# Optimization experiments

Hardware: AMD Instinct MI355X
Metric: run time of the kernel (lower is better)

The kernel has to match this reference:

```python
import jax, jax.numpy as jnp
import numpy as np

B, T, C, L = 128, 512, 1024, 64
BLANK = C - 1          # keras ctc_batch_cost uses last class as blank
NEG = -1e9             # finite log-zero (grad-safe)
EPS = 1e-7             # keras.backend.epsilon()


def setup_inputs() -> dict:
    key = jax.random.key(0)
    k1, k2, k3, k4 = jax.random.split(key, 4)
    # y_pred: softmax probabilities, as ctc_batch_cost expects
    y_pred = jax.nn.softmax(jax.random.normal(k1, (B, T, C), dtype=jnp.float32), axis=-1)
    y_true = jax.random.randint(k2, (B, L), 0, BLANK).astype(jnp.int32)  # labels exclude blank
    input_length = jax.random.randint(k3, (B, 1), T // 2, T + 1).astype(jnp.int32)
    label_length = jax.random.randint(k4, (B, 1), L // 2, L + 1).astype(jnp.int32)
    return {"y_true": y_true, "y_pred": y_pred,
            "input_length": input_length, "label_length": label_length}


def _lse3(a, b, c):
    m = jnp.maximum(jnp.maximum(a, b), c)
    return m + jnp.log(jnp.exp(a - m) + jnp.exp(b - m) + jnp.exp(c - m))


def _ctc_loss(y_pred, y_true, input_length, label_length):
    # log probs, exactly as keras: log(y_pred + epsilon)
    logp = jnp.log(y_pred + EPS)                     # [B,T,C]
    Bsz, Tmax, _ = logp.shape
    Lm = y_true.shape[1]
    S = 2 * Lm + 1                                   # extended label length

    # extended labels: blank at even positions, labels at odd
    lab_ext = jnp.full((Bsz, S), BLANK, dtype=y_true.dtype).at[:, 1::2].set(y_true)
    s_idx = jnp.arange(S)
    in_len = input_length.reshape(-1)                # [B]
    lab_len = label_length.reshape(-1)               # [B]
    valid = s_idx[None, :] < (2 * lab_len[:, None] + 1)

    # skip transition s-2 -> s allowed iff lab[s] != blank and lab[s] != lab[s-2]
    lab_m2 = jnp.concatenate(
        [jnp.full((Bsz, 2), -1, dtype=lab_ext.dtype), lab_ext[:, :-2]], axis=1)
    skip_ok = (s_idx[None, :] >= 2) & (lab_ext != BLANK) & (lab_ext != lab_m2)

    # virtual alpha_{-1}: mass only at position 0
    alpha0 = jnp.broadcast_to(jnp.where(s_idx == 0, 0.0, NEG), (Bsz, S)).astype(logp.dtype)

    def step(alpha, inputs):
        lp_t, t = inputs                              # lp_t: [B,C]
        emit = jnp.take_along_axis(lp_t, lab_ext, axis=1)           # [B,S]
        s1 = jnp.concatenate([jnp.full((Bsz, 1), NEG, logp.dtype), alpha[:, :-1]], axis=1)
        s2 = jnp.concatenate([jnp.full((Bsz, 2), NEG, logp.dtype), alpha[:, :-2]], axis=1)
        s2 = jnp.where(skip_ok, s2, NEG)
        a = emit + _lse3(alpha, s1, s2)
        a = jnp.where(valid, a, NEG)
        # freeze alpha once t >= input_length (per-example variable T)
        a = jnp.where((t < in_len)[:, None], a, alpha)
        return a, None

    lp_tb = jnp.transpose(logp, (1, 0, 2))            # [T,B,C]
    alpha_T, _ = jax.lax.scan(step, alpha0, (lp_tb, jnp.arange(Tmax)))

    end_blank = 2 * lab_len                           # index of final blank
    end_label = 2 * lab_len - 1                       # index of final label
    a1 = jnp.take_along_axis(alpha_T, end_blank[:, None], axis=1)[:, 0]
    a2 = jnp.take_along_axis(alpha_T, end_label[:, None], axis=1)[:, 0]
    loss = -jnp.logaddexp(a1, a2)                     # [B]
    return loss[:, None]                              # keras returns [B,1]


def reference(y_true, y_pred, input_length, label_length):
    return _ctc_loss(y_pred, y_true, input_length, label_length)
```

## Files before the change

kernel.cpp:

```cpp
#include <hip/hip_runtime.h>


constexpr int Tmax   = 512;
constexpr int Cch    = 1024;
constexpr int Lm     = 64;
constexpr int BLANKC = Cch - 1;
constexpr int ES     = 65;
constexpr int TS     = 8;
constexpr int PF2    = 8;

#define NEGF (-1e9f)
#define EPSF (1e-7f)
#define LN2F (0.69314718055994530942f)

__device__ __forceinline__ float wave_shr1(float src, float fill) {
    int r = __builtin_amdgcn_update_dpp(__float_as_int(fill), __float_as_int(src),
                                        0x138, 0xf, 0xf, false);
    return __int_as_float(r);
}
__device__ __forceinline__ float lae2(float a, float b) {
    float m = fmaxf(a, b);
    return m + __builtin_log2f(__builtin_exp2f(a - m) + __builtin_exp2f(b - m));
}
__device__ __forceinline__ float lse3_2(float a, float b, float c) {
    float m = fmaxf(fmaxf(a, b), c);
    return m + __builtin_log2f(__builtin_exp2f(a - m) +
                               __builtin_exp2f(b - m) +
                               __builtin_exp2f(c - m));
}
__device__ __forceinline__ int clampi(int v, int lo, int hi) {
    return v < lo ? lo : (v > hi ? hi : v);
}

__global__ __launch_bounds__(64, 1) void ctc_emit(
    const int*   __restrict__ y_true,
    const float* __restrict__ y_pred,
    const int*   __restrict__ in_len,
    float*       __restrict__ E)
{
    const int lane = threadIdx.x;
    const int b    = blockIdx.x;
    const int t0   = blockIdx.y * TS;

    const int Tb = clampi(in_len[b], 0, Tmax);
    if (t0 >= Tb) return;
    const int nt = (Tb - t0) < TS ? (Tb - t0) : TS;

    const int cls = y_true[b * Lm + lane];
    const float* __restrict__ base = y_pred + (size_t)b * Tmax * Cch;

    float pc[TS], pb[TS];
#pragma unroll
    for (int i = 0; i < TS; ++i) {
        const int t = t0 + (i < nt ? i : (nt - 1));
        const float* row = base + (size_t)t * Cch;
        pc[i] = row[cls];
        pb[i] = row[BLANKC];
    }
#pragma unroll
    for (int i = 0; i < TS; ++i) {
        if (i >= nt) break;
        const size_t idx = ((size_t)b * Tmax + (t0 + i)) * ES;
        E[idx + lane] = __builtin_log2f(pc[i] + EPSF);
        if (lane == 0) E[idx + 64] = __builtin_log2f(pb[i] + EPSF);
    }
}

__global__ __launch_bounds__(64, 1) void ctc_rec(
    const int*   __restrict__ y_true,
    const int*   __restrict__ in_len,
    const int*   __restrict__ lab_len,
    const float* __restrict__ E,
    float*       __restrict__ out)
{
    const int b    = blockIdx.x;
    const int lane = threadIdx.x;

    const int cls = y_true[b * Lm + lane];
    const int Tb  = clampi(in_len[b], 0, Tmax);
    const int lb  = clampi(lab_len[b], 0, Lm);

    const int  cls_prev = __shfl_up(cls, 1, 64);
    const bool skip     = (lane >= 1) && (cls != cls_prev);

    const bool val_lo = (lane <= lb);
    const bool val_hi = (lane <  lb);
    const bool val_ex = (lb == Lm);

    float a_lo = (lane == 0) ? 0.f : NEGF;
    float a_hi = NEGF;
    float a_ex = NEGF;

    const float* __restrict__ eb = E + (size_t)b * Tmax * ES;

    float pf_c[PF2], pf_b[PF2];
#pragma unroll
    for (int i = 0; i < PF2; ++i) {
        const float* row = eb + (size_t)i * ES;
        pf_c[i] = row[lane];
        pf_b[i] = row[64];
    }

    for (int t0 = 0; t0 < Tb; t0 += PF2) {
#pragma unroll
        for (int i = 0; i < PF2; ++i) {
            const int t = t0 + i;
            if (t >= Tb) break;

            const float e_c = pf_c[i];
            const float e_b = pf_b[i];

            {
                int tp = t + PF2; int tr = tp < Tmax ? tp : Tmax - 1;
                const float* row = eb + (size_t)tr * ES;
                pf_c[i] = row[lane];
                pf_b[i] = row[64];
            }

            const float p_hi = wave_shr1(a_hi, NEGF);

            float n_lo = e_b + lae2(a_lo, p_hi);
            float n_hi = e_c + lse3_2(a_hi, a_lo, skip ? p_hi : NEGF);
            float n_ex = e_b + lae2(a_ex, a_hi);

            a_lo = val_lo ? n_lo : NEGF;
            a_hi = val_hi ? n_hi : NEGF;
            a_ex = val_ex ? n_ex : NEGF;
        }
    }

    const float a_end_blank = (lb == Lm) ? __shfl(a_ex, 63, 64)
                                         : __shfl(a_lo, lb, 64);
    const int   el_lane     = (lb >= 1) ? (lb - 1) : 0;
    const float a_end_label = (lb >= 1) ? __shfl(a_hi, el_lane, 64)
                                        : __shfl(a_lo, 0, 64);

    if (lane == 0) {
        out[b] = -LN2F * lae2(a_end_blank, a_end_label);
    }
}

__global__ __launch_bounds__(64, 1) void ctc_fused(
    const int*   __restrict__ y_true,
    const float* __restrict__ y_pred,
    const int*   __restrict__ in_len,
    const int*   __restrict__ lab_len,
    float*       __restrict__ out)
{
    const int b    = blockIdx.x;
    const int lane = threadIdx.x;
    const int cls  = y_true[b * Lm + lane];
    const int Tb   = clampi(in_len[b], 0, Tmax);
    const int lb   = clampi(lab_len[b], 0, Lm);

    const int  cls_prev = __shfl_up(cls, 1, 64);
    const bool skip     = (lane >= 1) && (cls != cls_prev);
    const bool val_lo = (lane <= lb);
    const bool val_hi = (lane <  lb);
    const bool val_ex = (lb == Lm);

    float a_lo = (lane == 0) ? 0.f : NEGF;
    float a_hi = NEGF, a_ex = NEGF;
    const float* __restrict__ base = y_pred + (size_t)b * Tmax * Cch;

    constexpr int PF = 8;
    float pf_c[PF], pf_b[PF];
#pragma unroll
    for (int i = 0; i < PF; ++i) {
        const float* row = base + (size_t)i * Cch;
        pf_c[i] = row[cls]; pf_b[i] = row[BLANKC];
    }
    for (int t0 = 0; t0 < Tb; t0 += PF) {
#pragma unroll
        for (int i = 0; i < PF; ++i) {
            const int t = t0 + i;
            if (t >= Tb) break;
            const float e_c = __builtin_log2f(pf_c[i] + EPSF);
            const float e_b = __builtin_log2f(pf_b[i] + EPSF);
            { int tp = t + PF; int tr = tp < Tmax ? tp : Tmax - 1;
              const float* row = base + (size_t)tr * Cch;
              pf_c[i] = row[cls]; pf_b[i] = row[BLANKC]; }
            const float p_hi = wave_shr1(a_hi, NEGF);
            float n_lo = e_b + lae2(a_lo, p_hi);
            float n_hi = e_c + lse3_2(a_hi, a_lo, skip ? p_hi : NEGF);
            float n_ex = e_b + lae2(a_ex, a_hi);
            a_lo = val_lo ? n_lo : NEGF;
            a_hi = val_hi ? n_hi : NEGF;
            a_ex = val_ex ? n_ex : NEGF;
        }
    }
    const float a_end_blank = (lb == Lm) ? __shfl(a_ex, 63, 64)
                                         : __shfl(a_lo, lb, 64);
    const int   el_lane     = (lb >= 1) ? (lb - 1) : 0;
    const float a_end_label = (lb >= 1) ? __shfl(a_hi, el_lane, 64)
                                        : __shfl(a_lo, 0, 64);
    if (lane == 0) out[b] = -LN2F * lae2(a_end_blank, a_end_label);
}

extern "C" void kernel_launch(void* const* d_in, const int* in_sizes, int n_in,
                              void* d_out, int out_size, void* d_ws, size_t ws_size,
                              hipStream_t stream) {
    const int*   y_true  = (const int*)  d_in[0];
    const float* y_pred  = (const float*)d_in[1];
    const int*   in_len  = (const int*)  d_in[2];
    const int*   lab_len = (const int*)  d_in[3];
    float*       out     = (float*)      d_out;

    const size_t need = (size_t)128 * Tmax * ES * sizeof(float);
    if (ws_size >= need) {
        float* E = (float*)d_ws;
        ctc_emit<<<dim3(128, Tmax / TS), dim3(64), 0, stream>>>(
            y_true, y_pred, in_len, E);
        ctc_rec<<<dim3(128), dim3(64), 0, stream>>>(
            y_true, in_len, lab_len, E, out);
    } else {
        ctc_fused<<<dim3(128), dim3(64), 0, stream>>>(
            y_true, y_pred, in_len, lab_len, out);
    }
}
```

Baseline: 490.4 us.

## Stage full probability rows in LDS via coalesced float4 loads before gathering emissions

The emission-extraction kernel is replaced with a 256-thread kernel that handles 64 timesteps per block. Each wave streams whole 4KB rows of y_pred into its own LDS scratch with coalesced float4 loads, double-buffered in registers. It then gathers the label and blank probabilities from LDS instead of issuing scattered global loads. The emission row stride is padded from 65 to 66. This trades scattered gathers for full-row bandwidth and adds LDS traffic, while the serial recurrence kernel stays unchanged.

Result: slower. 598.8 us (+22.1%).

```diff
diff --git a/kernel.cpp b/kernel.cpp
--- a/kernel.cpp
+++ b/kernel.cpp
@@ -5,8 +5,8 @@
 constexpr int Cch    = 1024;
 constexpr int Lm     = 64;
 constexpr int BLANKC = Cch - 1;
-constexpr int ES     = 65;
-constexpr int TS     = 8;
+constexpr int ES     = 66;
+constexpr int CH     = 64;
 constexpr int PF2    = 8;
 
 #define NEGF (-1e9f)
@@ -32,37 +32,55 @@
     return v < lo ? lo : (v > hi ? hi : v);
 }
 
-__global__ __launch_bounds__(64, 1) void ctc_emit(
+__global__ __launch_bounds__(256, 1) void ctc_extract(
     const int*   __restrict__ y_true,
     const float* __restrict__ y_pred,
     const int*   __restrict__ in_len,
     float*       __restrict__ E)
 {
-    const int lane = threadIdx.x;
-    const int b    = blockIdx.x;
-    const int t0   = blockIdx.y * TS;
+    const int b     = blockIdx.x;
+    const int chunk = blockIdx.y;
+    const int wave  = threadIdx.x >> 6;
+    const int lane  = threadIdx.x & 63;
+
+    __shared__ float scr[4][Cch];
 
     const int Tb = clampi(in_len[b], 0, Tmax);
-    if (t0 >= Tb) return;
-    const int nt = (Tb - t0) < TS ? (Tb - t0) : TS;
+    const int nt = clampi(Tb - chunk * CH, 0, CH);
+    if (nt <= wave) return;
 
     const int cls = y_true[b * Lm + lane];
-    const float* __restrict__ base = y_pred + (size_t)b * Tmax * Cch;
-
-    float pc[TS], pb[TS];
-#pragma unroll
-    for (int i = 0; i < TS; ++i) {
-        const int t = t0 + (i < nt ? i : (nt - 1));
-        const float* row = base + (size_t)t * Cch;
-        pc[i] = row[cls];
-        pb[i] = row[BLANKC];
-    }
-#pragma unroll
-    for (int i = 0; i < TS; ++i) {
-        if (i >= nt) break;
-        const size_t idx = ((size_t)b * Tmax + (t0 + i)) * ES;
-        E[idx + lane] = __builtin_log2f(pc[i] + EPSF);
-        if (lane == 0) E[idx + 64] = __builtin_log2f(pb[i] + EPSF);
+    const float4* __restrict__ bv =
+        (const float4*)(y_pred + ((size_t)b * Tmax + chunk * CH) * Cch);
+    float4* __restrict__ s4 = (float4*)scr[wave];
+    float*  __restrict__ sd = scr[wave];
+
+    float4 nxt[4];
+#pragma unroll
+    for (int k = 0; k < 4; ++k)
+        nxt[k] = bv[(size_t)wave * 256 + k * 64 + lane];
+
+    for (int t = wave; t < nt; t += 4) {
+        float4 cur[4];
+#pragma unroll
+        for (int k = 0; k < 4; ++k) cur[k] = nxt[k];
+
+        const int tn = t + 4;
+        if (tn < nt) {
+#pragma unroll
+            for (int k = 0; k < 4; ++k)
+                nxt[k] = bv[(size_t)tn * 256 + k * 64 + lane];
+        }
+
+#pragma unroll
+        for (int k = 0; k < 4; ++k) s4[k * 64 + lane] = cur[k];
+
+        const float pc = sd[cls];
+        const float pb = sd[BLANKC];
+
+        const size_t e = ((size_t)b * Tmax + chunk * CH + t) * ES;
+        E[e + lane] = __builtin_log2f(pc + EPSF);
+        if (lane == 0) E[e + 64] = __builtin_log2f(pb + EPSF);
     }
 }
 
@@ -209,7 +227,7 @@
     const size_t need = (size_t)128 * Tmax * ES * sizeof(float);
     if (ws_size >= need) {
         float* E = (float*)d_ws;
-        ctc_emit<<<dim3(128, Tmax / TS), dim3(64), 0, stream>>>(
+        ctc_extract<<<dim3(128, Tmax / CH), dim3(256), 0, stream>>>(
             y_true, y_pred, in_len, E);
         ctc_rec<<<dim3(128), dim3(64), 0, stream>>>(
             y_true, in_len, lab_len, E, out);
```
